# Optimization experiments

Measured on AMD Instinct MI355X. Metric: run time of the kernel, lower is better.

## Reference

```python
import jax, jax.numpy as jnp
import numpy as np

B, S, H, D = 4, 1024, 32, 128   # batch, seq_len, heads, head_dim (prefill path, past_len=0)
HID = H * D                      # 4096
L, R = 8, 16                     # num_loras, lora rank
SCALE = 1.0 / float(np.sqrt(D))
LORA_SCALE = 1.0
ROPE_BASE = 10000.0


def setup_inputs() -> dict:
    key = jax.random.key(0)
    ks = jax.random.split(key, 16)
    T = B * S
    inp = {
        "x": jax.random.normal(ks[0], (T, HID), dtype=jnp.float32),
        "lora_idx": jax.random.randint(ks[1], (T,), 0, L, dtype=jnp.int32),
    }
    for i, n in enumerate(["Wq", "Wk", "Wv", "Wo"]):
        inp[n] = jax.random.normal(ks[2 + i], (HID, HID), dtype=jnp.float32) * 0.02
    for i, p in enumerate(["q", "k", "v", "o"]):
        inp[f"wa_{p}"] = jax.random.normal(ks[6 + 2 * i], (L, R, HID), dtype=jnp.float32) * 0.02
        inp[f"wb_{p}"] = jax.random.normal(ks[7 + 2 * i], (L, HID, R), dtype=jnp.float32) * 0.02
    return inp


def _add_lora(x, wa, wb, onehot):
    # punica bgmv: per-token lora: scale * (x @ A[idx]^T) @ B[idx]^T
    # Computed via one-hot selection to avoid materializing [T, O, R] gathers.
    a = jnp.einsum('th,lrh->tlr', x, wa)          # [T, L, R] (tiny)
    a_sel = jnp.einsum('tlr,tl->tr', a, onehot)   # [T, R]
    ar = jnp.einsum('tr,tl->tlr', a_sel, onehot)  # route back through lora slot
    return jnp.einsum('tlr,lor->to', ar, wb)      # [T, O]


def _rotary(x, cos, sin):
    # rotate_half over full head_dim: [-x2, x1]
    half = jnp.concatenate([-x[..., D // 2:], x[..., :D // 2]], axis=-1)
    return x * cos + half * sin


def reference(x, lora_idx, Wq, Wk, Wv, Wo,
              wa_q, wb_q, wa_k, wb_k, wa_v, wb_v, wa_o, wb_o):
    onehot = jax.nn.one_hot(lora_idx, L, dtype=x.dtype)  # [T, L]

    q = x @ Wq.T + LORA_SCALE * _add_lora(x, wa_q, wb_q, onehot)
    k = x @ Wk.T + LORA_SCALE * _add_lora(x, wa_k, wb_k, onehot)
    v = x @ Wv.T + LORA_SCALE * _add_lora(x, wa_v, wb_v, onehot)

    # [T, HID] -> [B, H, S, D]
    qh = q.reshape(B, S, H, D).transpose(0, 2, 1, 3)
    kh = k.reshape(B, S, H, D).transpose(0, 2, 1, 3)
    vh = v.reshape(B, S, H, D).transpose(0, 2, 1, 3)

    # rotary embedding, positions beg=past_len=0 .. S-1
    pos = jnp.arange(S, dtype=x.dtype)
    inv_freq = 1.0 / (ROPE_BASE ** (jnp.arange(0, D, 2, dtype=jnp.float32) / D)).astype(x.dtype)
    freqs = pos[:, None] * inv_freq[None, :]           # [S, D/2]
    emb = jnp.concatenate([freqs, freqs], axis=-1)     # [S, D]
    cos = jnp.cos(emb)[None, None]                     # [1,1,S,D]
    sin = jnp.sin(emb)[None, None]
    qh = _rotary(qh, cos, sin)
    kh = _rotary(kh, cos, sin)

    # causal SDPA
    scores = jnp.einsum('bhqd,bhkd->bhqk', qh, kh) * SCALE
    causal = jnp.tril(jnp.ones((S, S), dtype=bool))
    scores = jnp.where(causal[None, None], scores, jnp.finfo(scores.dtype).min)
    probs = jax.nn.softmax(scores, axis=-1)
    attn = jnp.einsum('bhqk,bhkd->bhqd', probs, vh)    # [B,H,S,D]
    attn = attn.transpose(0, 2, 1, 3).reshape(B * S, HID)

    out = attn @ Wo.T + LORA_SCALE * _add_lora(attn, wa_o, wb_o, onehot)
    return out
```

## Files before the change

### kernel.cpp

```cpp
#include <hip/hip_runtime.h>

#define HIDN 4096
#define KEXT 4224
#define TTOK 4096
#define SEQL 1024
#define NB 4
#define NHEAD 32
#define SCALEF 0.08838834764831845f

typedef __attribute__((ext_vector_type(8))) short bf16x8;
typedef __attribute__((ext_vector_type(8))) unsigned short u16x8;
typedef __attribute__((ext_vector_type(4))) float f32x4;

static __device__ __forceinline__ unsigned short f2bf(float f) {
  union { float f; unsigned u; } v; v.f = f;
  unsigned r = v.u + 0x7fffu + ((v.u >> 16) & 1u);
  return (unsigned short)(r >> 16);
}
static __device__ __forceinline__ void load_lds16(const void* g, void* l) {
  __builtin_amdgcn_global_load_lds((const __attribute__((address_space(1))) void*)g,
                                   (__attribute__((address_space(3))) void*)l, 16, 0, 0);
}

__global__ __launch_bounds__(256) void f2b_kernel(const float* __restrict__ s,
                                                  unsigned short* __restrict__ d) {
  size_t i = ((size_t)blockIdx.x * 256 + threadIdx.x) * 4;
  float4 v = *(const float4*)(s + i);
  ushort4 o;
  o.x = f2bf(v.x); o.y = f2bf(v.y); o.z = f2bf(v.z); o.w = f2bf(v.w);
  *(ushort4*)(d + i) = o;
}

__global__ __launch_bounds__(256) void f2b_pad_kernel(const float* __restrict__ s,
                                                      unsigned short* __restrict__ d) {
  size_t i = ((size_t)blockIdx.x * 256 + threadIdx.x) * 4;
  int row = (int)(i >> 12);
  int col = (int)(i & 4095);
  float4 v = *(const float4*)(s + i);
  ushort4 o;
  o.x = f2bf(v.x); o.y = f2bf(v.y); o.z = f2bf(v.z); o.w = f2bf(v.w);
  *(ushort4*)(d + (size_t)row * KEXT + col) = o;
}

__global__ __launch_bounds__(256) void wbbig_kernel(const float* __restrict__ wb,
                                                    unsigned short* __restrict__ wext) {
  int idx = blockIdx.x * 256 + threadIdx.x;
  int o = idx >> 5;
  int j4 = (idx & 31) * 4;
  int l = j4 >> 4, r = j4 & 15;
  float4 v = *(const float4*)(wb + ((size_t)l * HIDN + o) * 16 + r);
  ushort4 q;
  q.x = f2bf(v.x); q.y = f2bf(v.y); q.z = f2bf(v.z); q.w = f2bf(v.w);
  *(ushort4*)(wext + (size_t)o * KEXT + 4096 + j4) = q;
}

__global__ __launch_bounds__(128) void afat_kernel(const float* __restrict__ afull, int aoff,
    int awidth, const int* __restrict__ lidx, unsigned short* __restrict__ xext) {
  int t = blockIdx.x, j = threadIdx.x;
  int l = lidx[t];
  float v = afull[(size_t)t * awidth + aoff + j];
  unsigned short o = ((j >> 4) == l) ? f2bf(v) : (unsigned short)0;
  xext[(size_t)t * KEXT + 4096 + j] = o;
}

__global__ __launch_bounds__(256) void rope_tab_kernel(float* __restrict__ cosb,
                                                       float* __restrict__ sinb) {
  int i = blockIdx.x * 256 + threadIdx.x;
  int s = i >> 6, j = i & 63;
  float inv = __expf(-__logf(10000.0f) * (float)j * (1.0f / 64.0f));
  float f = (float)s * inv;
  cosb[i] = cosf(f);
  sinb[i] = sinf(f);
}

template<int BUF, bool ST>
__device__ __forceinline__ void ktile(char* lds, f32x4 (&acc)[8][4], int a_rd, int b_rd,
    const unsigned short* aS0, const unsigned short* aS1,
    const unsigned short* bS0, const unsigned short* bS1, int stg, int kn) {
  const int NB_ = (BUF ^ 1) * 32768;
  {
    __builtin_amdgcn_sched_barrier(0);
    bf16x8 af[4], bfr[4];
    #pragma unroll
    for (int mi = 0; mi < 4; ++mi)
      af[mi] = *(const bf16x8*)(lds + BUF * 32768 + a_rd + mi * 1024);
    #pragma unroll
    for (int ni = 0; ni < 4; ++ni)
      bfr[ni] = *(const bf16x8*)(lds + 65536 + BUF * 32768 + b_rd + ni * 1024);
    if (ST) {
      load_lds16(aS0 + kn, lds + NB_ + stg);
      load_lds16(aS1 + kn, lds + NB_ + stg + 1024);
    }
    __builtin_amdgcn_s_setprio(1);
    #pragma unroll
    for (int mi = 0; mi < 4; ++mi)
      #pragma unroll
      for (int ni = 0; ni < 4; ++ni)
        acc[mi][ni] = __builtin_amdgcn_mfma_f32_16x16x32_bf16(af[mi], bfr[ni], acc[mi][ni], 0, 0, 0);
    __builtin_amdgcn_s_setprio(0);
  }
  {
    __builtin_amdgcn_sched_barrier(0);
    bf16x8 af[4], bfr[4];
    #pragma unroll
    for (int mi = 0; mi < 4; ++mi)
      af[mi] = *(const bf16x8*)(lds + BUF * 32768 + 4096 + a_rd + mi * 1024);
    #pragma unroll
    for (int ni = 0; ni < 4; ++ni)
      bfr[ni] = *(const bf16x8*)(lds + 65536 + BUF * 32768 + b_rd + ni * 1024);
    if (ST) {
      load_lds16(bS0 + kn, lds + 65536 + NB_ + stg);
      load_lds16(bS1 + kn, lds + 65536 + NB_ + stg + 1024);
    }
    __builtin_amdgcn_s_setprio(1);
    #pragma unroll
    for (int mi = 0; mi < 4; ++mi)
      #pragma unroll
      for (int ni = 0; ni < 4; ++ni)
        acc[4 + mi][ni] = __builtin_amdgcn_mfma_f32_16x16x32_bf16(af[mi], bfr[ni], acc[4 + mi][ni], 0, 0, 0);
    __builtin_amdgcn_s_setprio(0);
  }
  if (ST) asm volatile("s_waitcnt vmcnt(4)" ::: "memory");
  else    asm volatile("s_waitcnt vmcnt(0)" ::: "memory");
  __builtin_amdgcn_s_barrier();
  {
    __builtin_amdgcn_sched_barrier(0);
    bf16x8 af[4], bfr[4];
    #pragma unroll
    for (int mi = 0; mi < 4; ++mi)
      af[mi] = *(const bf16x8*)(lds + BUF * 32768 + 16384 + a_rd + mi * 1024);
    #pragma unroll
    for (int ni = 0; ni < 4; ++ni)
      bfr[ni] = *(const bf16x8*)(lds + 65536 + BUF * 32768 + 16384 + b_rd + ni * 1024);
    if (ST) {
      load_lds16(aS0 + kn + 32, lds + NB_ + 16384 + stg);
      load_lds16(aS1 + kn + 32, lds + NB_ + 16384 + stg + 1024);
    }
    __builtin_amdgcn_s_setprio(1);
    #pragma unroll
    for (int mi = 0; mi < 4; ++mi)
      #pragma unroll
      for (int ni = 0; ni < 4; ++ni)
        acc[mi][ni] = __builtin_amdgcn_mfma_f32_16x16x32_bf16(af[mi], bfr[ni], acc[mi][ni], 0, 0, 0);
    __builtin_amdgcn_s_setprio(0);
  }
  {
    __builtin_amdgcn_sched_barrier(0);
    bf16x8 af[4], bfr[4];
    #pragma unroll
    for (int mi = 0; mi < 4; ++mi)
      af[mi] = *(const bf16x8*)(lds + BUF * 32768 + 16384 + 4096 + a_rd + mi * 1024);
    #pragma unroll
    for (int ni = 0; ni < 4; ++ni)
      bfr[ni] = *(const bf16x8*)(lds + 65536 + BUF * 32768 + 16384 + b_rd + ni * 1024);
    if (ST) {
      load_lds16(bS0 + kn + 32, lds + 65536 + NB_ + 16384 + stg);
      load_lds16(bS1 + kn + 32, lds + 65536 + NB_ + 16384 + stg + 1024);
    }
    __builtin_amdgcn_s_setprio(1);
    #pragma unroll
    for (int mi = 0; mi < 4; ++mi)
      #pragma unroll
      for (int ni = 0; ni < 4; ++ni)
        acc[4 + mi][ni] = __builtin_amdgcn_mfma_f32_16x16x32_bf16(af[mi], bfr[ni], acc[4 + mi][ni], 0, 0, 0);
    __builtin_amdgcn_s_setprio(0);
  }
  if (ST) {
    asm volatile("s_waitcnt vmcnt(4)" ::: "memory");
    __builtin_amdgcn_s_barrier();
  }
}

template<int KTOT>
__global__ __launch_bounds__(512, 2) void gemm256_kernel(const unsigned short* __restrict__ A,
    const unsigned short* __restrict__ Bw, float* __restrict__ C) {
  extern __shared__ char lds[];
  const int K = KTOT;
  int tid = threadIdx.x, lane = tid & 63, wave = tid >> 6;
  int wm = wave >> 2, wn = wave & 3;
  int l15 = lane & 15, l16 = lane >> 4;
  int orig = blockIdx.y * 16 + blockIdx.x;
  int swz = (orig & 7) * 32 + (orig >> 3);
  int bm = (swz >> 4) * 256, bn = (swz & 15) * 256;
  int srA0 = (wave * 2 + 0) * 16 + (lane >> 2);
  int srA1 = (wave * 2 + 1) * 16 + (lane >> 2);
  int scA0 = ((lane & 3) ^ ((srA0 >> 1) & 3)) * 8;
  int scA1 = ((lane & 3) ^ ((srA1 >> 1) & 3)) * 8;
  const unsigned short* aS0 = A + (size_t)(bm + srA0) * K + scA0;
  const unsigned short* aS1 = A + (size_t)(bm + srA1) * K + scA1;
  const unsigned short* bS0 = Bw + (size_t)(bn + srA0) * K + scA0;
  const unsigned short* bS1 = Bw + (size_t)(bn + srA1) * K + scA1;
  int stg = wave * 2048 + lane * 16;
  int rslot = (l16 ^ ((l15 >> 1) & 3)) * 16;
  int a_rd = (wm * 128 + l15) * 64 + rslot;
  int b_rd = (wn * 64 + l15) * 64 + rslot;
  f32x4 acc[8][4];
  const f32x4 fz = {0.f, 0.f, 0.f, 0.f};
  #pragma unroll
  for (int i = 0; i < 8; ++i)
    #pragma unroll
    for (int j = 0; j < 4; ++j) acc[i][j] = fz;
  load_lds16(aS0, lds + stg);
  load_lds16(aS1, lds + stg + 1024);
  load_lds16(bS0, lds + 65536 + stg);
  load_lds16(bS1, lds + 65536 + stg + 1024);
  load_lds16(aS0 + 32, lds + 16384 + stg);
  load_lds16(aS1 + 32, lds + 16384 + stg + 1024);
  load_lds16(bS0 + 32, lds + 65536 + 16384 + stg);
  load_lds16(bS1 + 32, lds + 65536 + 16384 + stg + 1024);
  asm volatile("s_waitcnt vmcnt(4)" ::: "memory");
  __builtin_amdgcn_s_barrier();
  for (int tt = 0; tt < KTOT / 128 - 1; ++tt) {
    ktile<0, true>(lds, acc, a_rd, b_rd, aS0, aS1, bS0, bS1, stg, (2 * tt + 1) * 64);
    ktile<1, true>(lds, acc, a_rd, b_rd, aS0, aS1, bS0, bS1, stg, (2 * tt + 2) * 64);
  }
  ktile<0, true>(lds, acc, a_rd, b_rd, aS0, aS1, bS0, bS1, stg, (KTOT / 64 - 1) * 64);
  ktile<1, false>(lds, acc, a_rd, b_rd, aS0, aS1, bS0, bS1, stg, 0);
  #pragma unroll
  for (int mi = 0; mi < 8; ++mi) {
    int gr = bm + wm * 128 + mi * 16 + l16 * 4;
    #pragma unroll
    for (int ni = 0; ni < 4; ++ni) {
      int gc = bn + wn * 64 + ni * 16 + l15;
      #pragma unroll
      for (int r = 0; r < 4; ++r)
        C[(size_t)(gr + r) * HIDN + gc] = acc[mi][ni][r];
    }
  }
}

__global__ __launch_bounds__(256) void gemm_bt_splitk_kernel(const unsigned short* __restrict__ A,
    const unsigned short* __restrict__ Bw, float* __restrict__ Cp, int N, int Ka) {
  __shared__ __align__(16) unsigned short As[128][32];
  __shared__ __align__(16) unsigned short Bs[128][32];
  const int KSPAN = 512;
  int tid = threadIdx.x;
  int lane = tid & 63, wave = tid >> 6;
  int bm = blockIdx.y * 128, bn = blockIdx.x * 128;
  int k0 = blockIdx.z * KSPAN;
  int wr = (wave >> 1) * 64, wc = (wave & 1) * 64;
  const f32x4 fz = {0.f, 0.f, 0.f, 0.f};
  f32x4 acc[4][4];
  #pragma unroll
  for (int i = 0; i < 4; ++i)
    #pragma unroll
    for (int j = 0; j < 4; ++j) acc[i][j] = fz;
  const unsigned short* a0 = A + (size_t)(bm + (tid >> 2)) * Ka + (tid & 3) * 8 + k0;
  const unsigned short* b0 = Bw + (size_t)(bn + (tid >> 2)) * HIDN + (tid & 3) * 8 + k0;
  char* lA = (char*)&As[0][0] + wave * 1024;
  char* lB = (char*)&Bs[0][0] + wave * 1024;
  int l15 = lane & 15, l4 = (lane >> 4) * 8;
  for (int kt = 0; kt < KSPAN; kt += 32) {
    load_lds16(a0 + kt, lA);
    load_lds16(a0 + kt + (size_t)64 * Ka, lA + 4096);
    load_lds16(b0 + kt, lB);
    load_lds16(b0 + kt + (size_t)64 * HIDN, lB + 4096);
    __syncthreads();
    bf16x8 af[4], bfr[4];
    #pragma unroll
    for (int mi = 0; mi < 4; ++mi) af[mi] = *(const bf16x8*)&As[wr + mi * 16 + l15][l4];
    #pragma unroll
    for (int ni = 0; ni < 4; ++ni) bfr[ni] = *(const bf16x8*)&Bs[wc + ni * 16 + l15][l4];
    #pragma unroll
    for (int mi = 0; mi < 4; ++mi)
      #pragma unroll
      for (int ni = 0; ni < 4; ++ni)
        acc[mi][ni] = __builtin_amdgcn_mfma_f32_16x16x32_bf16(af[mi], bfr[ni], acc[mi][ni], 0, 0, 0);
    __syncthreads();
  }
  float* Cz = Cp + (size_t)blockIdx.z * TTOK * N;
  #pragma unroll
  for (int mi = 0; mi < 4; ++mi) {
    int r0 = bm + wr + mi * 16 + (lane >> 4) * 4;
    #pragma unroll
    for (int ni = 0; ni < 4; ++ni) {
      int c = bn + wc + ni * 16 + l15;
      #pragma unroll
      for (int r = 0; r < 4; ++r)
        Cz[(size_t)(r0 + r) * N + c] = acc[mi][ni][r];
    }
  }
}

__global__ __launch_bounds__(256) void reduce8_kernel(const float* __restrict__ Cp,
                                                      float* __restrict__ C, int n) {
  int i = (blockIdx.x * 256 + threadIdx.x) * 4;
  float4 s = *(const float4*)(Cp + i);
  #pragma unroll
  for (int z = 1; z < 8; ++z) {
    float4 v = *(const float4*)(Cp + (size_t)z * n + i);
    s.x += v.x; s.y += v.y; s.z += v.z; s.w += v.w;
  }
  *(float4*)(C + i) = s;
}

__global__ __launch_bounds__(256) void finish_rope_kernel(const float* __restrict__ tmp,
    const float* __restrict__ cosb, const float* __restrict__ sinb,
    unsigned short* __restrict__ outb) {
  int t = blockIdx.x, tid = threadIdx.x;
  int c0 = tid * 16;
  const float* tr = tmp + (size_t)t * HIDN + c0;
  float vv[16];
  #pragma unroll
  for (int g = 0; g < 4; ++g) {
    float4 tv = *(const float4*)(tr + g * 4);
    vv[g * 4 + 0] = tv.x; vv[g * 4 + 1] = tv.y; vv[g * 4 + 2] = tv.z; vv[g * 4 + 3] = tv.w;
  }
  int s = t & (SEQL - 1);
  int jbase = (tid & 3) * 16;
  const float* cp = cosb + s * 64 + jbase;
  const float* sp = sinb + s * 64 + jbase;
  float cs[16], sn[16];
  #pragma unroll
  for (int g = 0; g < 4; ++g) {
    float4 c4 = *(const float4*)(cp + g * 4);
    float4 s4 = *(const float4*)(sp + g * 4);
    cs[g * 4] = c4.x; cs[g * 4 + 1] = c4.y; cs[g * 4 + 2] = c4.z; cs[g * 4 + 3] = c4.w;
    sn[g * 4] = s4.x; sn[g * 4 + 1] = s4.y; sn[g * 4 + 2] = s4.z; sn[g * 4 + 3] = s4.w;
  }
  bool lo = (tid & 4) == 0;
  #pragma unroll
  for (int j = 0; j < 16; ++j) {
    float pv = __shfl_xor(vv[j], 4, 64);
    vv[j] = lo ? (vv[j] * cs[j] - pv * sn[j]) : (vv[j] * cs[j] + pv * sn[j]);
  }
  unsigned short* op = outb + (size_t)t * HIDN + c0;
  u16x8 o0, o1;
  #pragma unroll
  for (int j = 0; j < 8; ++j) { o0[j] = f2bf(vv[j]); o1[j] = f2bf(vv[8 + j]); }
  *(u16x8*)op = o0;
  *(u16x8*)(op + 8) = o1;
}

__global__ __launch_bounds__(256) void attn_kernel(const unsigned short* __restrict__ qb,
    const unsigned short* __restrict__ kb, const unsigned short* __restrict__ vb,
    unsigned short* __restrict__ ob) {
  __shared__ __align__(16) unsigned short Ks[2][32][128];
  __shared__ __align__(16) unsigned short Vt[128][40];
  __shared__ __align__(16) unsigned short Ps[4][16][40];
  int tid = threadIdx.x, lane = tid & 63, wave = tid >> 6;
  int id = blockIdx.y * gridDim.x + blockIdx.x;
  int xcd = id & 7, w = id >> 3;
  int bh = xcd * 16 + (w & 15);
  int xp = w >> 4;
  int b = bh >> 5, h = bh & 31;
  size_t base = ((size_t)b * SEQL) * HIDN + (size_t)h * 128;
  size_t obase = ((size_t)b * SEQL) * KEXT + (size_t)h * 128;
  int l15 = lane & 15, l16 = lane >> 4;
  int krow = tid >> 4;
  int kslot = (tid & 15) ^ (krow & 7);
  const unsigned short* kgbase = kb + base + (size_t)krow * HIDN + kslot * 8;
  char* lK0 = (char*)&Ks[0][0][0] + wave * 1024;
  char* lK1 = (char*)&Ks[1][0][0] + wave * 1024;
  int vd = tid >> 1;
  int vks0 = (tid & 1) * 2;
  const unsigned short* vgbase = vb + base + vd;
  char* vtp = (char*)&Vt[0][0] + vd * 80 + vks0 * 16;
  const f32x4 fz = {0.f, 0.f, 0.f, 0.f};

  for (int half = 0; half < 2; ++half) {
    int qt = half ? (15 - xp) : xp;
    int q0 = qt * 64;
    int kend = q0 + 64;
    int qrow = q0 + wave * 16 + l15;
    const unsigned short* qrp = qb + base + (size_t)qrow * HIDN + l16 * 8;
    bf16x8 qf[4];
    #pragma unroll
    for (int ks = 0; ks < 4; ++ks) qf[ks] = *(const bf16x8*)(qrp + ks * 32);
    f32x4 oacc[8];
    #pragma unroll
    for (int i = 0; i < 8; ++i) oacc[i] = fz;
    float mrow[4] = {-1e30f, -1e30f, -1e30f, -1e30f};
    float lrow[4] = {0.f, 0.f, 0.f, 0.f};
    load_lds16(kgbase, lK0);
    load_lds16(kgbase + (size_t)16 * HIDN, lK0 + 4096);
    {
      bf16x8 v0, v1;
      const unsigned short* vg = vgbase + (size_t)(vks0 * 8) * HIDN;
      #pragma unroll
      for (int j = 0; j < 8; ++j) v0[j] = (short)vg[(size_t)j * HIDN];
      #pragma unroll
      for (int j = 0; j < 8; ++j) v1[j] = (short)vg[(size_t)(8 + j) * HIDN];
      *(bf16x8*)vtp = v0;
      *(bf16x8*)(vtp + 16) = v1;
    }
    __syncthreads();
    for (int kt = 0; kt < kend; kt += 32) {
      int cur = (kt >> 5) & 1;
      int more = (kt + 32) < kend;
      bf16x8 nv0, nv1;
      if (more) {
        char* lKn = cur ? lK0 : lK1;
        load_lds16(kgbase + (size_t)(kt + 32) * HIDN, lKn);
        load_lds16(kgbase + (size_t)(kt + 48) * HIDN, lKn + 4096);
        const unsigned short* vg = vgbase + (size_t)(kt + 32 + vks0 * 8) * HIDN;
        #pragma unroll
        for (int j = 0; j < 8; ++j) nv0[j] = (short)vg[(size_t)j * HIDN];
        #pragma unroll
        for (int j = 0; j < 8; ++j) nv1[j] = (short)vg[(size_t)(8 + j) * HIDN];
      }
      const char* ksb = (const char*)&Ks[cur][0][0];
      f32x4 sacc[2] = {fz, fz};
      #pragma unroll
      for (int ks = 0; ks < 4; ++ks) {
        #pragma unroll
        for (int nf = 0; nf < 2; ++nf) {
          int row = nf * 16 + l15;
          int slot = (ks * 4 + l16) ^ (l15 & 7);
          bf16x8 kf = *(const bf16x8*)(ksb + row * 256 + slot * 16);
          sacc[nf] = __builtin_amdgcn_mfma_f32_16x16x32_bf16(qf[ks], kf, sacc[nf], 0, 0, 0);
        }
      }
      float alpha[4];
      #pragma unroll
      for (int rr = 0; rr < 4; ++rr) {
        int qr = q0 + wave * 16 + l16 * 4 + rr;
        float s0 = sacc[0][rr], s1 = sacc[1][rr];
        if (kt + l15 > qr) s0 = -1e30f;
        if (kt + 16 + l15 > qr) s1 = -1e30f;
        float tm = fmaxf(s0, s1);
        #pragma unroll
        for (int off = 8; off > 0; off >>= 1) tm = fmaxf(tm, __shfl_xor(tm, off, 64));
        float mnew = fmaxf(mrow[rr], tm);
        float al = __expf(SCALEF * (mrow[rr] - mnew));
        float e0 = __expf(SCALEF * (s0 - mnew));
        float e1 = __expf(SCALEF * (s1 - mnew));
        float rs = e0 + e1;
        #pragma unroll
        for (int off = 8; off > 0; off >>= 1) rs += __shfl_xor(rs, off, 64);
        lrow[rr] = lrow[rr] * al + rs;
        mrow[rr] = mnew;
        alpha[rr] = al;
        Ps[wave][l16 * 4 + rr][l15] = f2bf(e0);
        Ps[wave][l16 * 4 + rr][16 + l15] = f2bf(e1);
      }
      #pragma unroll
      for (int nf = 0; nf < 8; ++nf) {
        #pragma unroll
        for (int rr = 0; rr < 4; ++rr) oacc[nf][rr] *= alpha[rr];
      }
      bf16x8 pf = *(const bf16x8*)&Ps[wave][l15][l16 * 8];
      #pragma unroll
      for (int nf = 0; nf < 8; ++nf) {
        bf16x8 vf = *(const bf16x8*)((const char*)&Vt[0][0] + (nf * 16 + l15) * 80 + l16 * 16);
        oacc[nf] = __builtin_amdgcn_mfma_f32_16x16x32_bf16(pf, vf, oacc[nf], 0, 0, 0);
      }
      __syncthreads();
      if (more) {
        *(bf16x8*)vtp = nv0;
        *(bf16x8*)(vtp + 16) = nv1;
      }
      __syncthreads();
    }
    #pragma unroll
    for (int rr = 0; rr < 4; ++rr) {
      int qr = q0 + wave * 16 + l16 * 4 + rr;
      float inv = 1.0f / lrow[rr];
      unsigned short* orow = ob + obase + (size_t)qr * KEXT;
      #pragma unroll
      for (int nf = 0; nf < 8; ++nf)
        orow[nf * 16 + l15] = f2bf(oacc[nf][rr] * inv);
    }
  }
}

extern "C" void kernel_launch(void* const* d_in, const int* in_sizes, int n_in,
                              void* d_out, int out_size, void* d_ws, size_t ws_size,
                              hipStream_t stream) {
  (void)in_sizes; (void)n_in; (void)out_size; (void)ws_size;
  const float* x = (const float*)d_in[0];
  const int* lidx = (const int*)d_in[1];
  const float* W[4] = {(const float*)d_in[2], (const float*)d_in[3],
                       (const float*)d_in[4], (const float*)d_in[5]};
  const float* wa_q = (const float*)d_in[6];
  const float* wb_q = (const float*)d_in[7];
  const float* wa_k = (const float*)d_in[8];
  const float* wb_k = (const float*)d_in[9];
  const float* wa_v = (const float*)d_in[10];
  const float* wb_v = (const float*)d_in[11];
  const float* wa_o = (const float*)d_in[12];
  const float* wb_o = (const float*)d_in[13];
  float* out = (float*)d_out;

  char* p = (char*)d_ws;
  unsigned short* Xext = (unsigned short*)p;  p += (size_t)TTOK * KEXT * 2;
  unsigned short* Wext = (unsigned short*)p;  p += (size_t)HIDN * KEXT * 2;
  float* tmp = (float*)p;                     p += (size_t)TTOK * HIDN * 4;
  unsigned short* qbuf = (unsigned short*)p;  p += (size_t)TTOK * HIDN * 2;
  unsigned short* kbuf = (unsigned short*)p;  p += (size_t)TTOK * HIDN * 2;
  unsigned short* vbuf = (unsigned short*)p;  p += (size_t)TTOK * HIDN * 2;
  unsigned short* Aext = (unsigned short*)p;  p += (size_t)TTOK * KEXT * 2;
  unsigned short* WAbf = (unsigned short*)p;  p += (size_t)384 * HIDN * 2;
  float* afull = (float*)p;                   p += (size_t)TTOK * 384 * 4;
  float* aofull = (float*)p;                  p += (size_t)TTOK * 128 * 4;
  float* cosb = (float*)p;                    p += (size_t)SEQL * 64 * 4;
  float* sinb = (float*)p;                    p += (size_t)SEQL * 64 * 4;

  const int CVT_BLOCKS = (TTOK * HIDN) / 1024;
  const int CVT_WA = (128 * HIDN) / 1024;
  const int WBBIG_BLOCKS = (HIDN * 32) / 256;
  dim3 g256(16, 16);

  hipFuncSetAttribute((const void*)gemm256_kernel<KEXT>,
                      hipFuncAttributeMaxDynamicSharedMemorySize, 131072);

  rope_tab_kernel<<<(SEQL * 64) / 256, 256, 0, stream>>>(cosb, sinb);
  f2b_pad_kernel<<<CVT_BLOCKS, 256, 0, stream>>>(x, Xext);
  f2b_kernel<<<CVT_WA, 256, 0, stream>>>(wa_q, WAbf);
  f2b_kernel<<<CVT_WA, 256, 0, stream>>>(wa_k, WAbf + (size_t)128 * HIDN);
  f2b_kernel<<<CVT_WA, 256, 0, stream>>>(wa_v, WAbf + (size_t)256 * HIDN);
  gemm_bt_splitk_kernel<<<dim3(3, 32, 8), 256, 0, stream>>>(Xext, WAbf, tmp, 384, KEXT);
  reduce8_kernel<<<(TTOK * 384) / 1024, 256, 0, stream>>>(tmp, afull, TTOK * 384);

  f2b_pad_kernel<<<CVT_BLOCKS, 256, 0, stream>>>(W[0], Wext);
  wbbig_kernel<<<WBBIG_BLOCKS, 256, 0, stream>>>(wb_q, Wext);
  afat_kernel<<<TTOK, 128, 0, stream>>>(afull, 0, 384, lidx, Xext);
  gemm256_kernel<KEXT><<<g256, 512, 131072, stream>>>(Xext, Wext, tmp);
  finish_rope_kernel<<<TTOK, 256, 0, stream>>>(tmp, cosb, sinb, qbuf);
  f2b_pad_kernel<<<CVT_BLOCKS, 256, 0, stream>>>(W[1], Wext);
  wbbig_kernel<<<WBBIG_BLOCKS, 256, 0, stream>>>(wb_k, Wext);
  afat_kernel<<<TTOK, 128, 0, stream>>>(afull, 128, 384, lidx, Xext);
  gemm256_kernel<KEXT><<<g256, 512, 131072, stream>>>(Xext, Wext, tmp);
  finish_rope_kernel<<<TTOK, 256, 0, stream>>>(tmp, cosb, sinb, kbuf);
  f2b_pad_kernel<<<CVT_BLOCKS, 256, 0, stream>>>(W[2], Wext);
  wbbig_kernel<<<WBBIG_BLOCKS, 256, 0, stream>>>(wb_v, Wext);
  afat_kernel<<<TTOK, 128, 0, stream>>>(afull, 256, 384, lidx, Xext);
  gemm256_kernel<KEXT><<<g256, 512, 131072, stream>>>(Xext, Wext, tmp);
  f2b_kernel<<<CVT_BLOCKS, 256, 0, stream>>>(tmp, vbuf);

  attn_kernel<<<dim3(SEQL / 128, NB * NHEAD), 256, 0, stream>>>(qbuf, kbuf, vbuf, Aext);

  f2b_kernel<<<CVT_WA, 256, 0, stream>>>(wa_o, WAbf);
  gemm_bt_splitk_kernel<<<dim3(1, 32, 8), 256, 0, stream>>>(Aext, WAbf, tmp, 128, KEXT);
  reduce8_kernel<<<(TTOK * 128) / 1024, 256, 0, stream>>>(tmp, aofull, TTOK * 128);
  f2b_pad_kernel<<<CVT_BLOCKS, 256, 0, stream>>>(W[3], Wext);
  wbbig_kernel<<<WBBIG_BLOCKS, 256, 0, stream>>>(wb_o, Wext);
  afat_kernel<<<TTOK, 128, 0, stream>>>(aofull, 0, 128, lidx, Aext);
  gemm256_kernel<KEXT><<<g256, 512, 131072, stream>>>(Aext, Wext, out);
}
```

Baseline: 944.1 us.

## Fuse RoPE and bf16 conversion into GEMM epilogue; compute softmax sum via MFMA

The GEMM's wave-to-column mapping is remapped so each wave holds both halves (d and d+64) of a head's rotary pair, which lets the Q/K projection epilogue apply RoPE and write bf16 directly. The V projection epilogue writes bf16 directly as well. This removes the fp32 tmp round trip and the separate finish_rope and f2b kernels. In attention, the per-row softmax denominator is now accumulated by an MFMA of P against a ones vector, replacing shuffle reductions. The cost is that the epilogue stores are scattered 2-byte writes and cos/sin are fetched per element. The row sum is also now taken over the bf16-rounded probabilities rather than the fp32 ones.

```diff
diff --git a/kernel.cpp b/kernel.cpp
--- a/kernel.cpp
+++ b/kernel.cpp
@@ -86,7 +86,7 @@
       af[mi] = *(const bf16x8*)(lds + BUF * 32768 + a_rd + mi * 1024);
     #pragma unroll
     for (int ni = 0; ni < 4; ++ni)
-      bfr[ni] = *(const bf16x8*)(lds + 65536 + BUF * 32768 + b_rd + ni * 1024);
+      bfr[ni] = *(const bf16x8*)(lds + 65536 + BUF * 32768 + b_rd + (ni & 1) * 1024 + (ni >> 1) * 4096);
     if (ST) {
       load_lds16(aS0 + kn, lds + NB_ + stg);
       load_lds16(aS1 + kn, lds + NB_ + stg + 1024);
@@ -107,7 +107,7 @@
       af[mi] = *(const bf16x8*)(lds + BUF * 32768 + 4096 + a_rd + mi * 1024);
     #pragma unroll
     for (int ni = 0; ni < 4; ++ni)
-      bfr[ni] = *(const bf16x8*)(lds + 65536 + BUF * 32768 + b_rd + ni * 1024);
+      bfr[ni] = *(const bf16x8*)(lds + 65536 + BUF * 32768 + b_rd + (ni & 1) * 1024 + (ni >> 1) * 4096);
     if (ST) {
       load_lds16(bS0 + kn, lds + 65536 + NB_ + stg);
       load_lds16(bS1 + kn, lds + 65536 + NB_ + stg + 1024);
@@ -131,7 +131,7 @@
       af[mi] = *(const bf16x8*)(lds + BUF * 32768 + 16384 + a_rd + mi * 1024);
     #pragma unroll
     for (int ni = 0; ni < 4; ++ni)
-      bfr[ni] = *(const bf16x8*)(lds + 65536 + BUF * 32768 + 16384 + b_rd + ni * 1024);
+      bfr[ni] = *(const bf16x8*)(lds + 65536 + BUF * 32768 + 16384 + b_rd + (ni & 1) * 1024 + (ni >> 1) * 4096);
     if (ST) {
       load_lds16(aS0 + kn + 32, lds + NB_ + 16384 + stg);
       load_lds16(aS1 + kn + 32, lds + NB_ + 16384 + stg + 1024);
@@ -152,7 +152,7 @@
       af[mi] = *(const bf16x8*)(lds + BUF * 32768 + 16384 + 4096 + a_rd + mi * 1024);
     #pragma unroll
     for (int ni = 0; ni < 4; ++ni)
-      bfr[ni] = *(const bf16x8*)(lds + 65536 + BUF * 32768 + 16384 + b_rd + ni * 1024);
+      bfr[ni] = *(const bf16x8*)(lds + 65536 + BUF * 32768 + 16384 + b_rd + (ni & 1) * 1024 + (ni >> 1) * 4096);
     if (ST) {
       load_lds16(bS0 + kn + 32, lds + 65536 + NB_ + 16384 + stg);
       load_lds16(bS1 + kn + 32, lds + 65536 + NB_ + 16384 + stg + 1024);
@@ -171,9 +171,10 @@
   }
 }
 
-template<int KTOT>
+template<int KTOT, int MODE>
 __global__ __launch_bounds__(512, 2) void gemm256_kernel(const unsigned short* __restrict__ A,
-    const unsigned short* __restrict__ Bw, float* __restrict__ C) {
+    const unsigned short* __restrict__ Bw, void* __restrict__ Cout,
+    const float* __restrict__ cosb, const float* __restrict__ sinb) {
   extern __shared__ char lds[];
   const int K = KTOT;
   int tid = threadIdx.x, lane = tid & 63, wave = tid >> 6;
@@ -193,7 +194,8 @@
   int stg = wave * 2048 + lane * 16;
   int rslot = (l16 ^ ((l15 >> 1) & 3)) * 16;
   int a_rd = (wm * 128 + l15) * 64 + rslot;
-  int b_rd = (wn * 64 + l15) * 64 + rslot;
+  int wcbase = (wn >> 1) * 128 + (wn & 1) * 32;
+  int b_rd = (wcbase + l15) * 64 + rslot;
   f32x4 acc[8][4];
   const f32x4 fz = {0.f, 0.f, 0.f, 0.f};
   #pragma unroll
@@ -216,15 +218,53 @@
   }
   ktile<0, true>(lds, acc, a_rd, b_rd, aS0, aS1, bS0, bS1, stg, (KTOT / 64 - 1) * 64);
   ktile<1, false>(lds, acc, a_rd, b_rd, aS0, aS1, bS0, bS1, stg, 0);
-  #pragma unroll
-  for (int mi = 0; mi < 8; ++mi) {
-    int gr = bm + wm * 128 + mi * 16 + l16 * 4;
-    #pragma unroll
-    for (int ni = 0; ni < 4; ++ni) {
-      int gc = bn + wn * 64 + ni * 16 + l15;
-      #pragma unroll
-      for (int r = 0; r < 4; ++r)
-        C[(size_t)(gr + r) * HIDN + gc] = acc[mi][ni][r];
+
+  if (MODE == 0) {
+    float* C = (float*)Cout;
+    #pragma unroll
+    for (int mi = 0; mi < 8; ++mi) {
+      int gr = bm + wm * 128 + mi * 16 + l16 * 4;
+      #pragma unroll
+      for (int ni = 0; ni < 4; ++ni) {
+        int gc = bn + wcbase + (ni & 1) * 16 + (ni >> 1) * 64 + l15;
+        #pragma unroll
+        for (int r = 0; r < 4; ++r)
+          C[(size_t)(gr + r) * HIDN + gc] = acc[mi][ni][r];
+      }
+    }
+  } else if (MODE == 2) {
+    unsigned short* O = (unsigned short*)Cout;
+    #pragma unroll
+    for (int mi = 0; mi < 8; ++mi) {
+      int gr = bm + wm * 128 + mi * 16 + l16 * 4;
+      #pragma unroll
+      for (int ni = 0; ni < 4; ++ni) {
+        int gc = bn + wcbase + (ni & 1) * 16 + (ni >> 1) * 64 + l15;
+        #pragma unroll
+        for (int r = 0; r < 4; ++r)
+          O[(size_t)(gr + r) * HIDN + gc] = f2bf(acc[mi][ni][r]);
+      }
+    }
+  } else {
+    unsigned short* O = (unsigned short*)Cout;
+    #pragma unroll
+    for (int mi = 0; mi < 8; ++mi) {
+      int gr = bm + wm * 128 + mi * 16 + l16 * 4;
+      #pragma unroll
+      for (int p = 0; p < 2; ++p) {
+        int jj = (wn & 1) * 32 + p * 16 + l15;
+        int gclo = bn + wcbase + p * 16 + l15;
+        #pragma unroll
+        for (int r = 0; r < 4; ++r) {
+          int row = gr + r;
+          int s = row & (SEQL - 1);
+          float cs = cosb[s * 64 + jj];
+          float sn = sinb[s * 64 + jj];
+          float lo = acc[mi][p][r], hi = acc[mi][p + 2][r];
+          O[(size_t)row * HIDN + gclo] = f2bf(lo * cs - hi * sn);
+          O[(size_t)row * HIDN + gclo + 64] = f2bf(hi * cs + lo * sn);
+        }
+      }
     }
   }
 }
@@ -292,44 +332,6 @@
     s.x += v.x; s.y += v.y; s.z += v.z; s.w += v.w;
   }
   *(float4*)(C + i) = s;
-}
-
-__global__ __launch_bounds__(256) void finish_rope_kernel(const float* __restrict__ tmp,
-    const float* __restrict__ cosb, const float* __restrict__ sinb,
-    unsigned short* __restrict__ outb) {
-  int t = blockIdx.x, tid = threadIdx.x;
-  int c0 = tid * 16;
-  const float* tr = tmp + (size_t)t * HIDN + c0;
-  float vv[16];
-  #pragma unroll
-  for (int g = 0; g < 4; ++g) {
-    float4 tv = *(const float4*)(tr + g * 4);
-    vv[g * 4 + 0] = tv.x; vv[g * 4 + 1] = tv.y; vv[g * 4 + 2] = tv.z; vv[g * 4 + 3] = tv.w;
-  }
-  int s = t & (SEQL - 1);
-  int jbase = (tid & 3) * 16;
-  const float* cp = cosb + s * 64 + jbase;
-  const float* sp = sinb + s * 64 + jbase;
-  float cs[16], sn[16];
-  #pragma unroll
-  for (int g = 0; g < 4; ++g) {
-    float4 c4 = *(const float4*)(cp + g * 4);
-    float4 s4 = *(const float4*)(sp + g * 4);
-    cs[g * 4] = c4.x; cs[g * 4 + 1] = c4.y; cs[g * 4 + 2] = c4.z; cs[g * 4 + 3] = c4.w;
-    sn[g * 4] = s4.x; sn[g * 4 + 1] = s4.y; sn[g * 4 + 2] = s4.z; sn[g * 4 + 3] = s4.w;
-  }
-  bool lo = (tid & 4) == 0;
-  #pragma unroll
-  for (int j = 0; j < 16; ++j) {
-    float pv = __shfl_xor(vv[j], 4, 64);
-    vv[j] = lo ? (vv[j] * cs[j] - pv * sn[j]) : (vv[j] * cs[j] + pv * sn[j]);
-  }
-  unsigned short* op = outb + (size_t)t * HIDN + c0;
-  u16x8 o0, o1;
-  #pragma unroll
-  for (int j = 0; j < 8; ++j) { o0[j] = f2bf(vv[j]); o1[j] = f2bf(vv[8 + j]); }
-  *(u16x8*)op = o0;
-  *(u16x8*)(op + 8) = o1;
 }
 
 __global__ __launch_bounds__(256) void attn_kernel(const unsigned short* __restrict__ qb,
@@ -357,6 +359,8 @@
   const unsigned short* vgbase = vb + base + vd;
   char* vtp = (char*)&Vt[0][0] + vd * 80 + vks0 * 16;
   const f32x4 fz = {0.f, 0.f, 0.f, 0.f};
+  const short ONEBF = (short)0x3F80;
+  const bf16x8 ones = {ONEBF, ONEBF, ONEBF, ONEBF, ONEBF, ONEBF, ONEBF, ONEBF};
 
   for (int half = 0; half < 2; ++half) {
     int qt = half ? (15 - xp) : xp;
@@ -370,8 +374,8 @@
     f32x4 oacc[8];
     #pragma unroll
     for (int i = 0; i < 8; ++i) oacc[i] = fz;
+    f32x4 sumac = fz;
     float mrow[4] = {-1e30f, -1e30f, -1e30f, -1e30f};
-    float lrow[4] = {0.f, 0.f, 0.f, 0.f};
     load_lds16(kgbase, lK0);
     load_lds16(kgbase + (size_t)16 * HIDN, lK0 + 4096);
     {
@@ -425,10 +429,6 @@
         float al = __expf(SCALEF * (mrow[rr] - mnew));
         float e0 = __expf(SCALEF * (s0 - mnew));
         float e1 = __expf(SCALEF * (s1 - mnew));
-        float rs = e0 + e1;
-        #pragma unroll
-        for (int off = 8; off > 0; off >>= 1) rs += __shfl_xor(rs, off, 64);
-        lrow[rr] = lrow[rr] * al + rs;
         mrow[rr] = mnew;
         alpha[rr] = al;
         Ps[wave][l16 * 4 + rr][l15] = f2bf(e0);
@@ -439,7 +439,10 @@
         #pragma unroll
         for (int rr = 0; rr < 4; ++rr) oacc[nf][rr] *= alpha[rr];
       }
+      #pragma unroll
+      for (int rr = 0; rr < 4; ++rr) sumac[rr] *= alpha[rr];
       bf16x8 pf = *(const bf16x8*)&Ps[wave][l15][l16 * 8];
+      sumac = __builtin_amdgcn_mfma_f32_16x16x32_bf16(pf, ones, sumac, 0, 0, 0);
       #pragma unroll
       for (int nf = 0; nf < 8; ++nf) {
         bf16x8 vf = *(const bf16x8*)((const char*)&Vt[0][0] + (nf * 16 + l15) * 80 + l16 * 16);
@@ -455,7 +458,7 @@
     #pragma unroll
     for (int rr = 0; rr < 4; ++rr) {
       int qr = q0 + wave * 16 + l16 * 4 + rr;
-      float inv = 1.0f / lrow[rr];
+      float inv = 1.0f / sumac[rr];
       unsigned short* orow = ob + obase + (size_t)qr * KEXT;
       #pragma unroll
       for (int nf = 0; nf < 8; ++nf)
@@ -501,7 +504,11 @@
   const int WBBIG_BLOCKS = (HIDN * 32) / 256;
   dim3 g256(16, 16);
 
-  hipFuncSetAttribute((const void*)gemm256_kernel<KEXT>,
+  hipFuncSetAttribute((const void*)gemm256_kernel<KEXT, 0>,
+                      hipFuncAttributeMaxDynamicSharedMemorySize, 131072);
+  hipFuncSetAttribute((const void*)gemm256_kernel<KEXT, 1>,
+                      hipFuncAttributeMaxDynamicSharedMemorySize, 131072);
+  hipFuncSetAttribute((const void*)gemm256_kernel<KEXT, 2>,
                       hipFuncAttributeMaxDynamicSharedMemorySize, 131072);
 
   rope_tab_kernel<<<(SEQL * 64) / 256, 256, 0, stream>>>(cosb, sinb);
@@ -515,18 +522,15 @@
   f2b_pad_kernel<<<CVT_BLOCKS, 256, 0, stream>>>(W[0], Wext);
   wbbig_kernel<<<WBBIG_BLOCKS, 256, 0, stream>>>(wb_q, Wext);
   afat_kernel<<<TTOK, 128, 0, stream>>>(afull, 0, 384, lidx, Xext);
-  gemm256_kernel<KEXT><<<g256, 512, 131072, stream>>>(Xext, Wext, tmp);
-  finish_rope_kernel<<<TTOK, 256, 0, stream>>>(tmp, cosb, sinb, qbuf);
+  gemm256_kernel<KEXT, 1><<<g256, 512, 131072, stream>>>(Xext, Wext, qbuf, cosb, sinb);
   f2b_pad_kernel<<<CVT_BLOCKS, 256, 0, stream>>>(W[1], Wext);
   wbbig_kernel<<<WBBIG_BLOCKS, 256, 0, stream>>>(wb_k, Wext);
   afat_kernel<<<TTOK, 128, 0, stream>>>(afull, 128, 384, lidx, Xext);
-  gemm256_kernel<KEXT><<<g256, 512, 131072, stream>>>(Xext, Wext, tmp);
-  finish_rope_kernel<<<TTOK, 256, 0, stream>>>(tmp, cosb, sinb, kbuf);
+  gemm256_kernel<KEXT, 1><<<g256, 512, 131072, stream>>>(Xext, Wext, kbuf, cosb, sinb);
   f2b_pad_kernel<<<CVT_BLOCKS, 256, 0, stream>>>(W[2], Wext);
   wbbig_kernel<<<WBBIG_BLOCKS, 256, 0, stream>>>(wb_v, Wext);
   afat_kernel<<<TTOK, 128, 0, stream>>>(afull, 256, 384, lidx, Xext);
-  gemm256_kernel<KEXT><<<g256, 512, 131072, stream>>>(Xext, Wext, tmp);
-  f2b_kernel<<<CVT_BLOCKS, 256, 0, stream>>>(tmp, vbuf);
+  gemm256_kernel<KEXT, 2><<<g256, 512, 131072, stream>>>(Xext, Wext, vbuf, nullptr, nullptr);
 
   attn_kernel<<<dim3(SEQL / 128, NB * NHEAD), 256, 0, stream>>>(qbuf, kbuf, vbuf, Aext);
 
@@ -536,5 +540,5 @@
   f2b_pad_kernel<<<CVT_BLOCKS, 256, 0, stream>>>(W[3], Wext);
   wbbig_kernel<<<WBBIG_BLOCKS, 256, 0, stream>>>(wb_o, Wext);
   afat_kernel<<<TTOK, 128, 0, stream>>>(aofull, 0, 128, lidx, Aext);
-  gemm256_kernel<KEXT><<<g256, 512, 131072, stream>>>(Aext, Wext, out);
-}
+  gemm256_kernel<KEXT, 0><<<g256, 512, 131072, stream>>>(Aext, Wext, out, nullptr, nullptr);
+}
```

Result: faster. 873.4 us (-7.5%).
